# Kernel optimization log

Hardware: AMD Instinct MI355X
Metric: run time of the kernel (lower is better)

## Reference

```python
import jax, jax.numpy as jnp
import numpy as np

HIDDEN = 4096
NUM_HEADS = 32
NUM_KV_HEADS = 8
HEAD_DIM = HIDDEN // NUM_HEADS  # 128
Q_SIZE = NUM_HEADS * HEAD_DIM    # 4096
KV_SIZE = NUM_KV_HEADS * HEAD_DIM  # 1024
SCALE = 1.0 / HEAD_DIM  # attention_multiplier=None -> head_dim ** (-1)
ROPE_BASE = 10000.0


def _rope_neox(x, positions):
    # x: [B, S, H, D], positions: [B, S] int
    half = HEAD_DIM // 2
    inv_freq = 1.0 / (ROPE_BASE ** (jnp.arange(0, half, dtype=jnp.float32) / half))
    freqs = positions.astype(jnp.float32)[..., None] * inv_freq  # [B, S, half]
    cos = jnp.cos(freqs)[:, :, None, :]  # [B, S, 1, half]
    sin = jnp.sin(freqs)[:, :, None, :]
    x1, x2 = x[..., :half], x[..., half:]
    return jnp.concatenate([x1 * cos - x2 * sin, x2 * cos + x1 * sin], axis=-1)


def setup_inputs() -> dict:
    key = jax.random.key(0)
    k1, k2, k3 = jax.random.split(key, 3)
    B, S = 2, 2048
    positions = jnp.broadcast_to(jnp.arange(S, dtype=jnp.int32), (B, S))
    hidden_states = jax.random.normal(k1, (B, S, HIDDEN), dtype=jnp.float32) * 0.02
    w_qkv = jax.random.normal(k2, (Q_SIZE + 2 * KV_SIZE, HIDDEN), dtype=jnp.float32) * 0.02
    w_o = jax.random.normal(k3, (HIDDEN, Q_SIZE), dtype=jnp.float32) * 0.02
    return {"positions": positions, "hidden_states": hidden_states, "w_qkv": w_qkv, "w_o": w_o}


def reference(positions, hidden_states, w_qkv, w_o):
    B, S, _ = hidden_states.shape
    # fused QKV projection
    qkv = jnp.einsum('bsh,oh->bso', hidden_states, w_qkv)
    q = qkv[..., :Q_SIZE].reshape(B, S, NUM_HEADS, HEAD_DIM)
    k = qkv[..., Q_SIZE:Q_SIZE + KV_SIZE].reshape(B, S, NUM_KV_HEADS, HEAD_DIM)
    v = qkv[..., Q_SIZE + KV_SIZE:].reshape(B, S, NUM_KV_HEADS, HEAD_DIM)
    # neox-style RoPE on q and k
    q = _rope_neox(q, positions)
    k = _rope_neox(k, positions)
    # GQA: repeat kv heads
    rep = NUM_HEADS // NUM_KV_HEADS
    k = jnp.repeat(k, rep, axis=2)  # [B, S, NUM_HEADS, D]
    v = jnp.repeat(v, rep, axis=2)
    # causal attention
    scores = jnp.einsum('bqhd,bkhd->bhqk', q, k) * SCALE
    causal = jnp.tril(jnp.ones((S, S), dtype=bool))
    scores = jnp.where(causal, scores, jnp.finfo(scores.dtype).min)
    probs = jax.nn.softmax(scores, axis=-1)
    attn = jnp.einsum('bhqk,bkhd->bqhd', probs, v).reshape(B, S, Q_SIZE)
    # output projection
    return jnp.einsum('bsq,hq->bsh', attn, w_o)
```

## Files before the change

kernel.cpp:

```cpp
#include <hip/hip_runtime.h>
#include <hip/hip_bf16.h>
#include <cmath>

typedef __bf16 bf16x8 __attribute__((ext_vector_type(8)));
typedef __bf16 bf16x4 __attribute__((ext_vector_type(4)));
typedef float  f32x4  __attribute__((ext_vector_type(4)));

#define AS1 __attribute__((address_space(1)))
#define AS3 __attribute__((address_space(3)))
#define GLDS16(gp, lp) __builtin_amdgcn_global_load_lds((AS1 void*)(gp), (AS3 void*)(lp), 16, 0, 0)

#define B_DIM 2
#define S_LEN 2048
#define HIDDEN 4096
#define NHEADS 32
#define NKV 8
#define HDIM 128
#define QSZ 4096
#define KVSZ 1024
#define QKVSZ 6144
#define GK 4096
#define ATT_SCALE 0.0078125f
#define L2E 1.4426950408889634f

__global__ __launch_bounds__(256) void conv_f32_bf16(const float* __restrict__ in,
                                                     __bf16* __restrict__ out, int n4) {
    int idx = blockIdx.x * 256 + threadIdx.x;
    if (idx < n4) {
        float4 v = ((const float4*)in)[idx];
        bf16x4 o;
        o[0] = (__bf16)v.x; o[1] = (__bf16)v.y; o[2] = (__bf16)v.z; o[3] = (__bf16)v.w;
        ((bf16x4*)out)[idx] = o;
    }
}

__global__ __launch_bounds__(256) void rope_table_kernel(float* __restrict__ ct,
                                                         float* __restrict__ st) {
    int idx = blockIdx.x * 256 + threadIdx.x;
    int p = idx >> 6, i = idx & 63;
    float inv = expf(-(float)i * (9.210340371976184f / 64.0f));
    float freq = (float)p * inv;
    float s, c;
    sincosf(freq, &s, &c);
    ct[idx] = c; st[idx] = s;
}

template<typename OUT>
__global__ __launch_bounds__(512, 2) void gemm256(const __bf16* __restrict__ A,
                                                  const __bf16* __restrict__ B,
                                                  OUT* __restrict__ C,
                                                  int N) {
    __shared__ __bf16 Asm[2 * 16384 + 2 * 16384];
    char* Bbase = (char*)Asm + 65536;

    const int tid = threadIdx.x;
    const int w = tid >> 6, l = tid & 63;
    const int l15 = l & 15, l4 = l >> 4;
    const int wr = w >> 2, wc = w & 3;

    const int nwg = gridDim.x * gridDim.y;
    const int orig = blockIdx.y * gridDim.x + blockIdx.x;
    const int swz = (orig & 7) * (nwg >> 3) + (orig >> 3);
    const int bx = swz % gridDim.x, by = swz / gridDim.x;
    const int m0 = by * 256, n0 = bx * 256;

    const __bf16* Ag = A + (size_t)m0 * GK;
    const __bf16* Bg = B + (size_t)n0 * GK;

#define STAGE_AQ(q, tile) do {                                                  \
        int c_ = (q) * 512 + tid;                                               \
        int r_ = c_ >> 3;                                                       \
        int jg_ = (tid & 7) ^ (r_ & 7);                                         \
        GLDS16(Ag + (size_t)r_ * GK + (tile) * 64 + jg_ * 8,                    \
               (char*)Asm + ((tile) & 1) * 32768 + c_ * 16);                    \
    } while (0)
#define STAGE_BS(s, tile) do {                                                  \
        _Pragma("unroll")                                                       \
        for (int i_ = 0; i_ < 2; ++i_) {                                        \
            int v_ = i_ * 512 + tid;                                            \
            int r_ = (v_ >> 8) * 64 + (s) * 32 + ((v_ >> 3) & 31);              \
            int jg_ = (v_ & 7) ^ (r_ & 7);                                      \
            int c_ = r_ * 8 + (v_ & 7);                                         \
            GLDS16(Bg + (size_t)r_ * GK + (tile) * 64 + jg_ * 8,                \
                   Bbase + ((tile) & 1) * 32768 + c_ * 16);                     \
        }                                                                       \
    } while (0)

#define LOAD_A(DST, MH) do {                                                    \
        _Pragma("unroll")                                                       \
        for (int m2 = 0; m2 < 4; ++m2) {                                        \
            int row = wr * 128 + ((MH) * 4 + m2) * 16 + l15;                    \
            _Pragma("unroll")                                                   \
            for (int kk = 0; kk < 2; ++kk) {                                    \
                int j = (kk * 4 + l4) ^ (row & 7);                              \
                DST[m2][kk] = *(const bf16x8*)(Als + row * 64 + j * 8);         \
            }                                                                   \
        }                                                                       \
    } while (0)
#define LOAD_B(DST, NH) do {                                                    \
        _Pragma("unroll")                                                       \
        for (int n2 = 0; n2 < 2; ++n2) {                                        \
            int row = wc * 64 + ((NH) * 2 + n2) * 16 + l15;                     \
            _Pragma("unroll")                                                   \
            for (int kk = 0; kk < 2; ++kk) {                                    \
                int j = (kk * 4 + l4) ^ (row & 7);                              \
                DST[n2][kk] = *(const bf16x8*)(Bls + row * 64 + j * 8);         \
            }                                                                   \
        }                                                                       \
    } while (0)
#define MFMA_QUAD(AF, BF, MI0, NI0)                                             \
    _Pragma("unroll")                                                           \
    for (int m2 = 0; m2 < 4; ++m2)                                              \
        _Pragma("unroll")                                                       \
        for (int n2 = 0; n2 < 2; ++n2)                                          \
            _Pragma("unroll")                                                   \
            for (int kk = 0; kk < 2; ++kk)                                      \
                acc[(MI0) + m2][(NI0) + n2] =                                   \
                    __builtin_amdgcn_mfma_f32_16x16x32_bf16(                    \
                        AF[m2][kk], BF[n2][kk], acc[(MI0) + m2][(NI0) + n2], 0, 0, 0);
#define PH_SYNC_PRE  do { __builtin_amdgcn_sched_barrier(0);                    \
        __builtin_amdgcn_s_barrier();                                           \
        asm volatile("s_waitcnt lgkmcnt(0)" ::: "memory");                      \
        __builtin_amdgcn_sched_barrier(0); } while (0)
#define PH_SYNC_POST do { __builtin_amdgcn_sched_barrier(0);                    \
        __builtin_amdgcn_s_barrier(); } while (0)

    f32x4 acc[8][4] = {};

    const int T = GK / 64;
    STAGE_AQ(0, 0); STAGE_AQ(1, 0); STAGE_AQ(2, 0); STAGE_AQ(3, 0);
    STAGE_BS(0, 0); STAGE_BS(1, 0);
    STAGE_AQ(0, 1); STAGE_AQ(2, 1); STAGE_BS(0, 1);
    asm volatile("s_waitcnt vmcnt(4)" ::: "memory");
    __builtin_amdgcn_s_barrier();

    for (int t = 0; t < T; ++t) {
        const __bf16* Als = Asm + (t & 1) * 16384;
        const __bf16* Bls = (__bf16*)Bbase + (t & 1) * 16384;
        bf16x8 af0[4][2], af1[4][2], bfr[2][2];
        LOAD_A(af0, 0);
        LOAD_B(bfr, 0);
        if (t + 1 < T) { STAGE_AQ(1, t + 1); STAGE_AQ(3, t + 1); }
        PH_SYNC_PRE;
        __builtin_amdgcn_s_setprio(1);
        MFMA_QUAD(af0, bfr, 0, 0);
        __builtin_amdgcn_s_setprio(0);
        PH_SYNC_POST;
        LOAD_B(bfr, 1);
        if (t + 1 < T) STAGE_BS(1, t + 1);
        PH_SYNC_PRE;
        __builtin_amdgcn_s_setprio(1);
        MFMA_QUAD(af0, bfr, 0, 2);
        __builtin_amdgcn_s_setprio(0);
        PH_SYNC_POST;
        LOAD_A(af1, 1);
        LOAD_B(bfr, 0);
        if (t + 2 < T) { STAGE_AQ(0, t + 2); STAGE_AQ(2, t + 2); }
        PH_SYNC_PRE;
        __builtin_amdgcn_s_setprio(1);
        MFMA_QUAD(af1, bfr, 4, 0);
        __builtin_amdgcn_s_setprio(0);
        PH_SYNC_POST;
        LOAD_B(bfr, 1);
        if (t + 2 < T) STAGE_BS(0, t + 2);
        PH_SYNC_PRE;
        __builtin_amdgcn_s_setprio(1);
        MFMA_QUAD(af1, bfr, 4, 2);
        __builtin_amdgcn_s_setprio(0);
        if (t + 2 < T)      { asm volatile("s_waitcnt vmcnt(4)" ::: "memory"); }
        else if (t + 1 < T) { asm volatile("s_waitcnt vmcnt(0)" ::: "memory"); }
        PH_SYNC_POST;
    }
#undef PH_SYNC_PRE
#undef PH_SYNC_POST
#undef MFMA_QUAD
#undef LOAD_A
#undef LOAD_B
#undef STAGE_AQ
#undef STAGE_BS

#pragma unroll
    for (int mi = 0; mi < 8; ++mi)
#pragma unroll
        for (int ni = 0; ni < 4; ++ni)
#pragma unroll
            for (int r = 0; r < 4; ++r)
                C[(size_t)(m0 + wr * 128 + mi * 16 + l4 * 4 + r) * N
                  + n0 + wc * 64 + ni * 16 + l15] = (OUT)acc[mi][ni][r];
}

__global__ __launch_bounds__(256) void rope_kernel(const __bf16* __restrict__ qkv,
                                                   const int* __restrict__ pos,
                                                   const float* __restrict__ ct,
                                                   const float* __restrict__ st,
                                                   __bf16* __restrict__ Qb,
                                                   __bf16* __restrict__ Kb) {
    const int tid = threadIdx.x;
    const int tok = blockIdx.x;
    const int b = tok >> 11, s = tok & 2047;
    const int p = pos[tok];
    const __bf16* base = qkv + (size_t)tok * QKVSZ;
    const float* cb = ct + (size_t)p * 64;
    const float* sb = st + (size_t)p * 64;
    for (int idx = tid; idx < 2560; idx += 256) {
        int head = idx >> 6, i = idx & 63;
        float c = cb[i], sn = sb[i];
        if (head < 32) {
            float x1 = (float)base[head * HDIM + i];
            float x2 = (float)base[head * HDIM + 64 + i];
            size_t o = ((size_t)(b * 32 + head) * S_LEN + s) * HDIM + i;
            Qb[o]      = (__bf16)((x1 * c - x2 * sn) * ATT_SCALE);
            Qb[o + 64] = (__bf16)((x2 * c + x1 * sn) * ATT_SCALE);
        } else {
            int g = head - 32;
            float x1 = (float)base[QSZ + g * HDIM + i];
            float x2 = (float)base[QSZ + g * HDIM + 64 + i];
            size_t o = ((size_t)(b * 8 + g) * S_LEN + s) * HDIM + i;
            Kb[o]      = (__bf16)(x1 * c - x2 * sn);
            Kb[o + 64] = (__bf16)(x2 * c + x1 * sn);
        }
    }
}

__global__ __launch_bounds__(256) void vtrans_kernel(const __bf16* __restrict__ qkv,
                                                     __bf16* __restrict__ Vt) {
    __shared__ __bf16 T[64][132];
    const int tid = threadIdx.x;
    const int st = blockIdx.x, g = blockIdx.y, b = blockIdx.z;
    const __bf16* src = qkv + ((size_t)(b * S_LEN + st * 64)) * QKVSZ + (QSZ + KVSZ) + g * HDIM;
#pragma unroll
    for (int it = 0; it < 8; ++it) {
        int c = it * 256 + tid;
        int row = c >> 5;
        int c4 = c & 31;
        bf16x4 v = *(const bf16x4*)(src + (size_t)row * QKVSZ + c4 * 4);
        *(bf16x4*)(&T[row][c4 * 4]) = v;
    }
    __syncthreads();
#pragma unroll
    for (int it = 0; it < 8; ++it) {
        int c = it * 256 + tid;
        int d = c >> 4;
        int s4 = (c & 15) * 4;
        bf16x4 o;
        o[0] = T[s4 + 0][d]; o[1] = T[s4 + 1][d]; o[2] = T[s4 + 2][d]; o[3] = T[s4 + 3][d];
        *(bf16x4*)(Vt + ((size_t)(b * 8 + g) * HDIM + d) * S_LEN + st * 64 + s4) = o;
    }
}

__global__ __launch_bounds__(256, 2) void attn_kernel(const __bf16* __restrict__ Q,
                                                      const __bf16* __restrict__ K,
                                                      const __bf16* __restrict__ Vt,
                                                      __bf16* __restrict__ O) {
    const int tid = threadIdx.x;
    const int w = tid >> 6, l = tid & 63;
    const int l15 = l & 15, l4 = l >> 4;
    const int qt = gridDim.x - 1 - blockIdx.x;
    const int h = blockIdx.y, b = blockIdx.z;
    const int g = h >> 2;
    const int qw0 = qt * 128 + w * 32;

    __shared__ __bf16 Ks[2][64 * 128];
    __shared__ __bf16 Vs[2][128 * 64];
    __shared__ __bf16 Pl[4 * 32 * 64];

    const __bf16* Qp = Q + ((size_t)((b * 32 + h) * S_LEN + qw0)) * HDIM;
    const __bf16* Kp = K + (size_t)(b * 8 + g) * S_LEN * HDIM;
    const __bf16* Vp = Vt + (size_t)(b * 8 + g) * HDIM * S_LEN;

    bf16x8 qf[2][4];
#pragma unroll
    for (int qh = 0; qh < 2; ++qh)
#pragma unroll
        for (int kk = 0; kk < 4; ++kk)
            qf[qh][kk] = *(const bf16x8*)(Qp + (size_t)(qh * 16 + l15) * HDIM + kk * 32 + l4 * 8);

    f32x4 acc[2][8] = {};
    float m[2]    = {-1e30f, -1e30f};
    float lsum[2] = {0.f, 0.f};

#define STAGE(buf, ktile) do {                                                     \
        const __bf16* kbase = Kp + (size_t)(ktile) * 64 * HDIM;                    \
        _Pragma("unroll")                                                          \
        for (int i_ = 0; i_ < 4; ++i_) {                                           \
            int c_ = i_ * 256 + tid;                \
            int row_ = c_ >> 4, cc_ = (c_ & 15) ^ (row_ & 7);                      \
            GLDS16(kbase + (size_t)row_ * HDIM + cc_ * 8,                          \
                   (char*)Ks[buf] + c_ * 16);                                      \
        }                                                                          \
        const __bf16* vbase = Vp + (size_t)(ktile) * 64;                           \
        _Pragma("unroll")                                                          \
        for (int i_ = 0; i_ < 4; ++i_) {                                           \
            int c_ = i_ * 256 + tid;                \
            int row_ = c_ >> 3, cc_ = (c_ & 7) ^ (row_ & 7);                       \
            GLDS16(vbase + (size_t)row_ * S_LEN + cc_ * 8,                         \
                   (char*)Vs[buf] + c_ * 16);                                      \
        }                                                                          \
    } while (0)

    const int nkt = 2 * qt + 2;
    int cur = 0;
    STAGE(0, 0);
    __syncthreads();

    for (int kt = 0; kt < nkt; ++kt) {
        if (kt + 1 < nkt) STAGE(cur ^ 1, kt + 1);
        if (kt * 64 <= qw0 + 31) {
            f32x4 sfr[2][4];
            __builtin_amdgcn_s_setprio(1);
#pragma unroll
            for (int fn = 0; fn < 4; ++fn) {
                f32x4 sa0 = {}, sa1 = {};
#pragma unroll
                for (int kk = 0; kk < 4; ++kk) {
                    int row = fn * 16 + l15;
                    int cc = (kk * 4 + l4) ^ (l15 & 7);
                    bf16x8 kb = *(const bf16x8*)(Ks[cur] + row * HDIM + cc * 8);
                    sa0 = __builtin_amdgcn_mfma_f32_16x16x32_bf16(kb, qf[0][kk], sa0, 0, 0, 0);
                    sa1 = __builtin_amdgcn_mfma_f32_16x16x32_bf16(kb, qf[1][kk], sa1, 0, 0, 0);
                }
                sfr[0][fn] = sa0; sfr[1][fn] = sa1;
            }
            __builtin_amdgcn_s_setprio(0);
            const bool needmask = (kt * 64 + 63 > qw0);
#pragma unroll
            for (int qh = 0; qh < 2; ++qh) {
                const int qrow = qw0 + qh * 16 + l15;
                float pmax = -1e30f;
#pragma unroll
                for (int fn = 0; fn < 4; ++fn)
#pragma unroll
                    for (int r = 0; r < 4; ++r) {
                        float v = sfr[qh][fn][r];
                        if (needmask) {
                            int kcol = kt * 64 + fn * 16 + l4 * 4 + r;
                            if (kcol > qrow) v = -1e30f;
                        }
                        sfr[qh][fn][r] = v;
                        pmax = fmaxf(pmax, v);
                    }
                pmax = fmaxf(pmax, __shfl_xor(pmax, 16));
                pmax = fmaxf(pmax, __shfl_xor(pmax, 32));
                if (!__all(pmax - m[qh] <= 8.0f)) {
                    float mn = fmaxf(m[qh], pmax);
                    float alpha = exp2f((m[qh] - mn) * L2E);
                    m[qh] = mn;
                    lsum[qh] *= alpha;
#pragma unroll
                    for (int r = 0; r < 4; ++r) {
                        float ar = __shfl(alpha, l4 * 4 + r, 16);
#pragma unroll
                        for (int n = 0; n < 8; ++n) acc[qh][n][r] *= ar;
                    }
                }
                float rs = 0.f;
#pragma unroll
                for (int fn = 0; fn < 4; ++fn) {
                    bf16x4 pk;
#pragma unroll
                    for (int r = 0; r < 4; ++r) {
                        float p = exp2f((sfr[qh][fn][r] - m[qh]) * L2E);
                        rs += p;
                        pk[r] = (__bf16)p;
                    }
                    *(bf16x4*)(Pl + w * 2048 + (qh * 16 + l15) * 64
                               + (((fn * 4 + l4) ^ ((l15 & 3) << 2)) * 4)) = pk;
                }
                rs += __shfl_xor(rs, 16);
                rs += __shfl_xor(rs, 32);
                lsum[qh] += rs;
            }
            asm volatile("s_waitcnt lgkmcnt(0)" ::: "memory");
            __builtin_amdgcn_sched_barrier(0);
            __builtin_amdgcn_s_setprio(1);
#pragma unroll
            for (int kk = 0; kk < 2; ++kk) {
                int pc = ((kk * 8 + l4 * 2) ^ ((l15 & 3) << 2)) * 4;
                bf16x8 pa0 = *(const bf16x8*)(Pl + w * 2048 + l15 * 64 + pc);
                bf16x8 pa1 = *(const bf16x8*)(Pl + w * 2048 + (16 + l15) * 64 + pc);
#pragma unroll
                for (int n = 0; n < 8; ++n) {
                    int row = n * 16 + l15;
                    int cc = (kk * 4 + l4) ^ (l15 & 7);
                    bf16x8 vb = *(const bf16x8*)(Vs[cur] + row * 64 + cc * 8);
                    acc[0][n] = __builtin_amdgcn_mfma_f32_16x16x32_bf16(pa0, vb, acc[0][n], 0, 0, 0);
                    acc[1][n] = __builtin_amdgcn_mfma_f32_16x16x32_bf16(pa1, vb, acc[1][n], 0, 0, 0);
                }
            }
            __builtin_amdgcn_s_setprio(0);
        }
        __syncthreads();
        cur ^= 1;
    }
#undef STAGE
#pragma unroll
    for (int qh = 0; qh < 2; ++qh)
#pragma unroll
        for (int r = 0; r < 4; ++r) {
            float inv = 1.0f / __shfl(lsum[qh], l4 * 4 + r, 16);
            int row = qw0 + qh * 16 + l4 * 4 + r;
#pragma unroll
            for (int n = 0; n < 8; ++n)
                O[((size_t)(b * S_LEN) + row) * QSZ + h * HDIM + n * 16 + l15] = (__bf16)(acc[qh][n][r] * inv);
        }
}

extern "C" void kernel_launch(void* const* d_in, const int* in_sizes, int n_in,
                              void* d_out, int out_size, void* d_ws, size_t ws_size,
                              hipStream_t stream) {
    const int*   pos    = (const int*)d_in[0];
    const float* hidden = (const float*)d_in[1];
    const float* wqkv   = (const float*)d_in[2];
    const float* wo     = (const float*)d_in[3];
    float* out = (float*)d_out;

    __bf16* hb    = (__bf16*)d_ws;
    __bf16* wqb   = hb  + 16777216;
    __bf16* wob   = wqb + 25165824;
    __bf16* qkv   = wob + 16777216;
    __bf16* Qb    = qkv + 25165824;
    __bf16* Kb    = Qb  + 16777216;
    __bf16* Vtb   = Kb  + 4194304;
    __bf16* attnb = Vtb + 4194304;
    float*  rc    = (float*)(attnb + 16777216);
    float*  rs    = rc + 131072;

    conv_f32_bf16<<<16384, 256, 0, stream>>>(hidden, hb, 4194304);
    conv_f32_bf16<<<24576, 256, 0, stream>>>(wqkv, wqb, 6291456);
    conv_f32_bf16<<<16384, 256, 0, stream>>>(wo, wob, 4194304);
    rope_table_kernel<<<512, 256, 0, stream>>>(rc, rs);
    gemm256<__bf16><<<dim3(QKVSZ / 256, (B_DIM * S_LEN) / 256), 512, 0, stream>>>(hb, wqb, qkv, QKVSZ);
    rope_kernel<<<B_DIM * S_LEN, 256, 0, stream>>>(qkv, pos, rc, rs, Qb, Kb);
    vtrans_kernel<<<dim3(S_LEN / 64, NKV, B_DIM), 256, 0, stream>>>(qkv, Vtb);
    attn_kernel<<<dim3(S_LEN / 128, NHEADS, B_DIM), 256, 0, stream>>>(Qb, Kb, Vtb, attnb);
    gemm256<float><<<dim3(HIDDEN / 256, (B_DIM * S_LEN) / 256), 512, 0, stream>>>(attnb, wob, out, HIDDEN);
}
```

Measured before the change: 617.7 us.

## Keep softmax probabilities in registers via permlane swaps instead of LDS round-trip

The attention kernel stops writing the probability tile P to shared memory and reading it back for the PV matmul. It now packs P to bf16 with v_cvt_pk_bf16_f32 and rearranges it across lanes with v_permlane32_swap plus xor shuffles. The PV MFMA operands are swapped (V as A, P as B), so the accumulator is transposed: each lane now holds one query row. That lets the rescale use a per-lane alpha and the final store write contiguous bf16x4 vectors. This removes LDS traffic, the lgkmcnt wait and a sched barrier, but adds cross-lane permute and shuffle instructions and depends on the lane mapping being exactly right.

Measured after the change: 625.6 us. No clear change (+1.3%).

```diff
diff --git a/kernel.cpp b/kernel.cpp
--- a/kernel.cpp
+++ b/kernel.cpp
@@ -5,6 +5,8 @@
 typedef __bf16 bf16x8 __attribute__((ext_vector_type(8)));
 typedef __bf16 bf16x4 __attribute__((ext_vector_type(4)));
 typedef float  f32x4  __attribute__((ext_vector_type(4)));
+typedef unsigned int u32;
+typedef u32 u32x4 __attribute__((ext_vector_type(4)));
 
 #define AS1 __attribute__((address_space(1)))
 #define AS3 __attribute__((address_space(3)))
@@ -262,7 +264,6 @@
 
     __shared__ __bf16 Ks[2][64 * 128];
     __shared__ __bf16 Vs[2][128 * 64];
-    __shared__ __bf16 Pl[4 * 32 * 64];
 
     const __bf16* Qp = Q + ((size_t)((b * 32 + h) * S_LEN + qw0)) * HDIM;
     const __bf16* Kp = K + (size_t)(b * 8 + g) * S_LEN * HDIM;
@@ -278,6 +279,7 @@
     f32x4 acc[2][8] = {};
     float m[2]    = {-1e30f, -1e30f};
     float lsum[2] = {0.f, 0.f};
+    const bool oddl4 = (l4 & 1);
 
 #define STAGE(buf, ktile) do {                                                     \
         const __bf16* kbase = Kp + (size_t)(ktile) * 64 * HDIM;                    \
@@ -323,6 +325,7 @@
             }
             __builtin_amdgcn_s_setprio(0);
             const bool needmask = (kt * 64 + 63 > qw0);
+            bf16x8 pb[2][2];
 #pragma unroll
             for (int qh = 0; qh < 2; ++qh) {
                 const int qrow = qw0 + qh * 16 + l15;
@@ -347,44 +350,53 @@
                     m[qh] = mn;
                     lsum[qh] *= alpha;
 #pragma unroll
-                    for (int r = 0; r < 4; ++r) {
-                        float ar = __shfl(alpha, l4 * 4 + r, 16);
-#pragma unroll
-                        for (int n = 0; n < 8; ++n) acc[qh][n][r] *= ar;
-                    }
+                    for (int n = 0; n < 8; ++n)
+#pragma unroll
+                        for (int r = 0; r < 4; ++r) acc[qh][n][r] *= alpha;
                 }
                 float rs = 0.f;
+                u32 pk01[4], pk23[4];
 #pragma unroll
                 for (int fn = 0; fn < 4; ++fn) {
-                    bf16x4 pk;
-#pragma unroll
-                    for (int r = 0; r < 4; ++r) {
-                        float p = exp2f((sfr[qh][fn][r] - m[qh]) * L2E);
-                        rs += p;
-                        pk[r] = (__bf16)p;
-                    }
-                    *(bf16x4*)(Pl + w * 2048 + (qh * 16 + l15) * 64
-                               + (((fn * 4 + l4) ^ ((l15 & 3) << 2)) * 4)) = pk;
+                    float p0 = exp2f((sfr[qh][fn][0] - m[qh]) * L2E);
+                    float p1 = exp2f((sfr[qh][fn][1] - m[qh]) * L2E);
+                    float p2 = exp2f((sfr[qh][fn][2] - m[qh]) * L2E);
+                    float p3 = exp2f((sfr[qh][fn][3] - m[qh]) * L2E);
+                    rs += (p0 + p1) + (p2 + p3);
+                    asm("v_cvt_pk_bf16_f32 %0, %1, %2" : "=v"(pk01[fn]) : "v"(p0), "v"(p1));
+                    asm("v_cvt_pk_bf16_f32 %0, %1, %2" : "=v"(pk23[fn]) : "v"(p2), "v"(p3));
                 }
                 rs += __shfl_xor(rs, 16);
                 rs += __shfl_xor(rs, 32);
                 lsum[qh] += rs;
+#pragma unroll
+                for (int kk = 0; kk < 2; ++kk) {
+                    u32 a01 = pk01[2 * kk],     a23 = pk23[2 * kk];
+                    u32 b01 = pk01[2 * kk + 1], b23 = pk23[2 * kk + 1];
+                    asm("v_permlane32_swap_b32 %0, %1" : "+v"(a01), "+v"(b01));
+                    asm("v_permlane32_swap_b32 %0, %1" : "+v"(a23), "+v"(b23));
+                    u32 oa01 = __shfl_xor(a01, 16);
+                    u32 oa23 = __shfl_xor(a23, 16);
+                    u32 ob01 = __shfl_xor(b01, 16);
+                    u32 ob23 = __shfl_xor(b23, 16);
+                    u32x4 wv;
+                    wv[0] = oddl4 ? ob01 : a01;
+                    wv[1] = oddl4 ? ob23 : a23;
+                    wv[2] = oddl4 ? b01 : oa01;
+                    wv[3] = oddl4 ? b23 : oa23;
+                    pb[qh][kk] = __builtin_bit_cast(bf16x8, wv);
+                }
             }
-            asm volatile("s_waitcnt lgkmcnt(0)" ::: "memory");
-            __builtin_amdgcn_sched_barrier(0);
             __builtin_amdgcn_s_setprio(1);
 #pragma unroll
             for (int kk = 0; kk < 2; ++kk) {
-                int pc = ((kk * 8 + l4 * 2) ^ ((l15 & 3) << 2)) * 4;
-                bf16x8 pa0 = *(const bf16x8*)(Pl + w * 2048 + l15 * 64 + pc);
-                bf16x8 pa1 = *(const bf16x8*)(Pl + w * 2048 + (16 + l15) * 64 + pc);
 #pragma unroll
                 for (int n = 0; n < 8; ++n) {
                     int row = n * 16 + l15;
                     int cc = (kk * 4 + l4) ^ (l15 & 7);
                     bf16x8 vb = *(const bf16x8*)(Vs[cur] + row * 64 + cc * 8);
-                    acc[0][n] = __builtin_amdgcn_mfma_f32_16x16x32_bf16(pa0, vb, acc[0][n], 0, 0, 0);
-                    acc[1][n] = __builtin_amdgcn_mfma_f32_16x16x32_bf16(pa1, vb, acc[1][n], 0, 0, 0);
+                    acc[0][n] = __builtin_amdgcn_mfma_f32_16x16x32_bf16(vb, pb[0][kk], acc[0][n], 0, 0, 0);
+                    acc[1][n] = __builtin_amdgcn_mfma_f32_16x16x32_bf16(vb, pb[1][kk], acc[1][n], 0, 0, 0);
                 }
             }
             __builtin_amdgcn_s_setprio(0);
@@ -394,15 +406,18 @@
     }
 #undef STAGE
 #pragma unroll
-    for (int qh = 0; qh < 2; ++qh)
-#pragma unroll
-        for (int r = 0; r < 4; ++r) {
-            float inv = 1.0f / __shfl(lsum[qh], l4 * 4 + r, 16);
-            int row = qw0 + qh * 16 + l4 * 4 + r;
-#pragma unroll
-            for (int n = 0; n < 8; ++n)
-                O[((size_t)(b * S_LEN) + row) * QSZ + h * HDIM + n * 16 + l15] = (__bf16)(acc[qh][n][r] * inv);
+    for (int qh = 0; qh < 2; ++qh) {
+        float inv = 1.0f / lsum[qh];
+        int qrow = qw0 + qh * 16 + l15;
+        __bf16* obase = O + ((size_t)(b * S_LEN) + qrow) * QSZ + h * HDIM + l4 * 4;
+#pragma unroll
+        for (int n = 0; n < 8; ++n) {
+            bf16x4 o4;
+#pragma unroll
+            for (int r = 0; r < 4; ++r) o4[r] = (__bf16)(acc[qh][n][r] * inv);
+            *(bf16x4*)(obase + n * 16) = o4;
         }
+    }
 }
 
 extern "C" void kernel_launch(void* const* d_in, const int* in_sizes, int n_in,
```
